# Performance work log

Measured on AMD Instinct MI355X. Metric: run time of the kernel, lower is better.

Reference implementation:

```python
import jax, jax.numpy as jnp
import numpy as np

# NF4 codebook (bitsandbytes values)
NF4_LEVELS = jnp.array([-1.0, -0.6961928009986877, -0.5250730514526367, -0.39491748809814453,
                        -0.28444138169288635, -0.18477343022823334, -0.09105003625154495, 0.0,
                        0.07958029955625534, 0.16093020141124725, 0.24611230194568634,
                        0.33791524171829224, 0.44070982933044434, 0.5626170039176941,
                        0.7229568362236023, 1.0], dtype=jnp.float32)

IN_FEATURES = 4096
OUT_FEATURES = 4096


def setup_inputs() -> dict:
    key = jax.random.key(0)
    k1, k2, k3, k4 = jax.random.split(key, 4)
    x = jax.random.normal(k1, (4, 2048, IN_FEATURES), dtype=jnp.float32)
    # packed uint8 bytes (stored as int32 in [0,256)), shape (O, I//2)
    packed = jax.random.randint(k2, (OUT_FEATURES, IN_FEATURES // 2), 0, 256, dtype=jnp.int32)
    absmax = jax.random.uniform(k3, (OUT_FEATURES,), dtype=jnp.float32) + 1e-3
    bias = jax.random.normal(k4, (OUT_FEATURES,), dtype=jnp.float32)
    return {"x": x, "packed": packed, "absmax": absmax, "bias": bias}


def dequantize_nf4(packed, absmax):
    # packed: (O, I//2) int bytes; high nibble first, then low nibble
    high = (packed >> 4) & 15
    low = packed & 15
    idx = jnp.stack([high, low], axis=2).reshape(packed.shape[0], -1)  # (O, I)
    w = NF4_LEVELS[idx]                    # LUT dequant, (O, I)
    return w * absmax[:, None]             # per-row absmax scaling


def reference(x, packed, absmax, bias):
    # forward: dequantize weight on-the-fly, then F.linear(x, W, bias)
    w = dequantize_nf4(packed, absmax)     # (O, I)
    return jnp.einsum('bsi,oi->bso', x, w) + bias
```

## Files before the change

### kernel.cpp

```cpp
#include <hip/hip_runtime.h>
#include <hip/hip_bf16.h>
#include <stdint.h>

#define M_DIM 8192
#define N_DIM 4096
#define K_DIM 4096

typedef __bf16 bf16_t;
typedef __attribute__((ext_vector_type(8))) __bf16 bf16x8;
typedef __attribute__((ext_vector_type(4))) __bf16 bf16x4;
typedef __attribute__((ext_vector_type(4))) float f32x4;

__constant__ float NF4_LUT[16] = {
    -1.0f, -0.6961928009986877f, -0.5250730514526367f, -0.39491748809814453f,
    -0.28444138169288635f, -0.18477343022823334f, -0.09105003625154495f, 0.0f,
    0.07958029955625534f, 0.16093020141124725f, 0.24611230194568634f,
    0.33791524171829224f, 0.44070982933044434f, 0.5626170039176941f,
    0.7229568362236023f, 1.0f};

__global__ __launch_bounds__(256) void dequant_nf4_kernel(
    const int* __restrict__ packed, const float* __restrict__ absmax,
    bf16_t* __restrict__ W) {
  const int t = blockIdx.x * 256 + threadIdx.x;
  const int row = t >> 9;
  const int c = t & 511;
  const int lane = threadIdx.x & 63;
  const int lutbits = __float_as_int(NF4_LUT[lane & 15]);

  const int4 p = ((const int4*)packed)[t];
  const float am = absmax[row];
  bf16x8 v;
#pragma unroll
  for (int q = 0; q < 4; ++q) {
    const int byte = (q == 0 ? p.x : q == 1 ? p.y : q == 2 ? p.z : p.w) & 255;
    const float hi =
        __int_as_float(__builtin_amdgcn_ds_bpermute(((byte >> 4) & 15) << 2, lutbits));
    const float lo =
        __int_as_float(__builtin_amdgcn_ds_bpermute((byte & 15) << 2, lutbits));
    v[2 * q] = (bf16_t)(hi * am);
    v[2 * q + 1] = (bf16_t)(lo * am);
  }
  *((bf16x8*)&W[(size_t)row * K_DIM + c * 8]) = v;
}

__global__ __launch_bounds__(256) void cvt_bf16_kernel(
    const float* __restrict__ x, bf16_t* __restrict__ y) {
  const int t = blockIdx.x * 256 + threadIdx.x;
  const float4 a = ((const float4*)x)[t];
  bf16x4 v;
  v[0] = (bf16_t)a.x; v[1] = (bf16_t)a.y; v[2] = (bf16_t)a.z; v[3] = (bf16_t)a.w;
  *((bf16x4*)&y[(size_t)t * 4]) = v;
}

#define GLD_LDS16(g, l)                                                     \
  __builtin_amdgcn_global_load_lds(                                        \
      (const __attribute__((address_space(1))) void*)(g),                   \
      (__attribute__((address_space(3))) void*)(l), 16, 0, 0)

__global__ __launch_bounds__(256) void gemm_nf4_kernel(
    const bf16_t* __restrict__ A, const bf16_t* __restrict__ B,
    const float* __restrict__ bias, float* __restrict__ C) {
  constexpr int BM = 128, BN = 128, BK = 32;
  __shared__ __align__(16) bf16_t sA[BM * BK];
  __shared__ __align__(16) bf16_t sB[BN * BK];

  const int tid = threadIdx.x;
  const int wave = tid >> 6, lane = tid & 63;
  const int wr = wave >> 1, wc = wave & 1;
  const int quad = lane >> 4, l15 = lane & 15;

  const int blockM = blockIdx.y * BM;
  const int blockN = blockIdx.x * BN;

  const int sr = tid >> 2;
  const int sk = ((tid & 3) ^ ((tid >> 3) & 3)) * 8;
  const bf16_t* gA0 = A + (size_t)(blockM + sr) * K_DIM + sk;
  const bf16_t* gA1 = gA0 + (size_t)64 * K_DIM;
  const bf16_t* gB0 = B + (size_t)(blockN + sr) * K_DIM + sk;
  const bf16_t* gB1 = gB0 + (size_t)64 * K_DIM;
  bf16_t* lA0 = &sA[tid * 8];
  bf16_t* lA1 = &sA[(tid + 256) * 8];
  bf16_t* lB0 = &sB[tid * 8];
  bf16_t* lB1 = &sB[(tid + 256) * 8];

  f32x4 acc[4][4];
#pragma unroll
  for (int i = 0; i < 4; ++i)
#pragma unroll
    for (int j = 0; j < 4; ++j) acc[i][j] = (f32x4)(0.0f);

  const int cphys = quad ^ ((l15 >> 1) & 3);

  for (int k0 = 0; k0 < K_DIM; k0 += BK) {
    GLD_LDS16(gA0 + k0, lA0);
    GLD_LDS16(gA1 + k0, lA1);
    GLD_LDS16(gB0 + k0, lB0);
    GLD_LDS16(gB1 + k0, lB1);
    __syncthreads();

    bf16x8 af[4], bfr[4];
#pragma unroll
    for (int i = 0; i < 4; ++i) {
      const int rr = wr * 64 + i * 16 + l15;
      af[i] = *(const bf16x8*)&sA[(rr * 4 + cphys) * 8];
    }
#pragma unroll
    for (int j = 0; j < 4; ++j) {
      const int rr = wc * 64 + j * 16 + l15;
      bfr[j] = *(const bf16x8*)&sB[(rr * 4 + cphys) * 8];
    }

#pragma unroll
    for (int i = 0; i < 4; ++i)
#pragma unroll
      for (int j = 0; j < 4; ++j)
        acc[i][j] = __builtin_amdgcn_mfma_f32_16x16x32_bf16(af[i], bfr[j],
                                                            acc[i][j], 0, 0, 0);
    __syncthreads();
  }

#pragma unroll
  for (int j = 0; j < 4; ++j) {
    const int n = blockN + wc * 64 + j * 16 + l15;
    const float bv = bias[n];
#pragma unroll
    for (int i = 0; i < 4; ++i) {
      const int m0 = blockM + wr * 64 + i * 16 + quad * 4;
      f32x4 v = acc[i][j];
      C[(size_t)(m0 + 0) * N_DIM + n] = v[0] + bv;
      C[(size_t)(m0 + 1) * N_DIM + n] = v[1] + bv;
      C[(size_t)(m0 + 2) * N_DIM + n] = v[2] + bv;
      C[(size_t)(m0 + 3) * N_DIM + n] = v[3] + bv;
    }
  }
}

__global__ __launch_bounds__(256) void fallback_kernel(
    const float* __restrict__ x, const int* __restrict__ packed,
    const float* __restrict__ absmax, const float* __restrict__ bias,
    float* __restrict__ out) {
  const int idx = blockIdx.x * 256 + threadIdx.x;
  const int m = idx / N_DIM, n = idx % N_DIM;
  const int* prow = packed + (size_t)n * (K_DIM / 2);
  const float* xr = x + (size_t)m * K_DIM;
  float s = 0.0f;
  for (int p = 0; p < K_DIM / 2; ++p) {
    const int b = prow[p] & 255;
    s += xr[2 * p] * NF4_LUT[(b >> 4) & 15] + xr[2 * p + 1] * NF4_LUT[b & 15];
  }
  out[idx] = s * absmax[n] + bias[n];
}

extern "C" void kernel_launch(void* const* d_in, const int* in_sizes, int n_in,
                              void* d_out, int out_size, void* d_ws,
                              size_t ws_size, hipStream_t stream) {
  const float* x = (const float*)d_in[0];
  const int* packed = (const int*)d_in[1];
  const float* absmax = (const float*)d_in[2];
  const float* bias = (const float*)d_in[3];
  float* out = (float*)d_out;

  const size_t wBytes = (size_t)N_DIM * K_DIM * sizeof(bf16_t);
  const size_t xBytes = (size_t)M_DIM * K_DIM * sizeof(bf16_t);
  if (ws_size < wBytes + xBytes) {
    fallback_kernel<<<dim3((M_DIM * N_DIM) / 256), dim3(256), 0, stream>>>(
        x, packed, absmax, bias, out);
    return;
  }

  bf16_t* W = (bf16_t*)d_ws;
  bf16_t* xb = (bf16_t*)((char*)d_ws + wBytes);

  dequant_nf4_kernel<<<dim3((N_DIM * (K_DIM / 2) / 4) / 256), dim3(256), 0,
                       stream>>>(packed, absmax, W);
  cvt_bf16_kernel<<<dim3((M_DIM * K_DIM / 4) / 256), dim3(256), 0, stream>>>(
      x, xb);
  gemm_nf4_kernel<<<dim3(N_DIM / 128, M_DIM / 128), dim3(256), 0, stream>>>(
      xb, W, bias, out);
}
```

Measured before the change: 543.0 us.

## Rewrite GEMM as 256x256 tile, 8-wave, double-buffered LDS pipeline

Replaces the 128x128x32 single-buffer GEMM with a 256x256x64 tile on 512 threads (8 waves, 2x4 layout). LDS is double-buffered: half-tiles for step t+1 and t+2 are prefetched with global_load_lds while the MFMAs work on the current tile, and the phases are separated by explicit barriers, waitcnts and setprio. It also adds a grouped block-index remap for L2 locality and XOR swizzling of LDS. The aim is to hide load latency and raise arithmetic intensity per tile. In exchange it uses 128KB of LDS, more registers (128 accumulators per lane), and fragile hand-tuned synchronisation.

Result: faster. 527.9 us (-2.8%).

```diff
diff --git a/kernel.cpp b/kernel.cpp
--- a/kernel.cpp
+++ b/kernel.cpp
@@ -57,76 +57,205 @@
       (const __attribute__((address_space(1))) void*)(g),                   \
       (__attribute__((address_space(3))) void*)(l), 16, 0, 0)
 
-__global__ __launch_bounds__(256) void gemm_nf4_kernel(
+#define MFMA_BF16(a, b, c) \
+  __builtin_amdgcn_mfma_f32_16x16x32_bf16((a), (b), (c), 0, 0, 0)
+
+#define STAGE_A1(tt, lds)                                    \
+  do {                                                       \
+    GLD_LDS16(gA1a + (size_t)(tt) * 64, (lds) + dA0);        \
+    GLD_LDS16(gA1b + (size_t)(tt) * 64, (lds) + dA0 + 16384);\
+  } while (0)
+#define STAGE_A2(tt, lds)                                    \
+  do {                                                       \
+    GLD_LDS16(gA2a + (size_t)(tt) * 64, (lds) + dA0 + 8192); \
+    GLD_LDS16(gA2b + (size_t)(tt) * 64, (lds) + dA0 + 24576);\
+  } while (0)
+#define STAGE_B1(tt, lds)                                    \
+  do {                                                       \
+    GLD_LDS16(gB1a + (size_t)(tt) * 64, (lds) + dB0);        \
+    GLD_LDS16(gB1b + (size_t)(tt) * 64, (lds) + dB0 + 16384);\
+  } while (0)
+#define STAGE_B2(tt, lds)                                    \
+  do {                                                       \
+    GLD_LDS16(gB2a + (size_t)(tt) * 64, (lds) + dB0 + 4096); \
+    GLD_LDS16(gB2b + (size_t)(tt) * 64, (lds) + dB0 + 20480);\
+  } while (0)
+
+#define END_BARRIER()                \
+  asm volatile("" ::: "memory");     \
+  __builtin_amdgcn_s_barrier();      \
+  asm volatile("" ::: "memory")
+
+#define MID_BARRIER()                                   \
+  asm volatile("" ::: "memory");                        \
+  __builtin_amdgcn_s_barrier();                         \
+  asm volatile("s_waitcnt lgkmcnt(0)" ::: "memory");    \
+  __builtin_amdgcn_sched_barrier(0)
+
+__global__ __launch_bounds__(512, 2) void gemm_nf4_kernel(
     const bf16_t* __restrict__ A, const bf16_t* __restrict__ B,
     const float* __restrict__ bias, float* __restrict__ C) {
-  constexpr int BM = 128, BN = 128, BK = 32;
-  __shared__ __align__(16) bf16_t sA[BM * BK];
-  __shared__ __align__(16) bf16_t sB[BN * BK];
+  constexpr int NT = K_DIM / 64;
+  __shared__ __align__(16) bf16_t sA[2][256 * 64];
+  __shared__ __align__(16) bf16_t sB[2][256 * 64];
 
   const int tid = threadIdx.x;
   const int wave = tid >> 6, lane = tid & 63;
-  const int wr = wave >> 1, wc = wave & 1;
-  const int quad = lane >> 4, l15 = lane & 15;
-
-  const int blockM = blockIdx.y * BM;
-  const int blockN = blockIdx.x * BN;
-
-  const int sr = tid >> 2;
-  const int sk = ((tid & 3) ^ ((tid >> 3) & 3)) * 8;
-  const bf16_t* gA0 = A + (size_t)(blockM + sr) * K_DIM + sk;
-  const bf16_t* gA1 = gA0 + (size_t)64 * K_DIM;
-  const bf16_t* gB0 = B + (size_t)(blockN + sr) * K_DIM + sk;
-  const bf16_t* gB1 = gB0 + (size_t)64 * K_DIM;
-  bf16_t* lA0 = &sA[tid * 8];
-  bf16_t* lA1 = &sA[(tid + 256) * 8];
-  bf16_t* lB0 = &sB[tid * 8];
-  bf16_t* lB1 = &sB[(tid + 256) * 8];
-
-  f32x4 acc[4][4];
-#pragma unroll
-  for (int i = 0; i < 4; ++i)
+  const int wm = wave >> 2, wn = wave & 3;
+  const int quad = lane >> 4, l15 = lane & 15, l7 = lane & 7;
+
+  const int id = (blockIdx.x & 7) * 64 + (blockIdx.x >> 3);
+  const int blockM = (id & 31) * 256;
+  const int blockN = (id >> 5) * 256;
+
+  const int rqa = tid >> 3;
+  const int cira = ((tid & 7) ^ (rqa & 7)) * 8;
+  const bf16_t* gA1a = A + (size_t)(blockM + rqa) * K_DIM + cira;
+  const bf16_t* gA1b = gA1a + (size_t)128 * K_DIM;
+  const bf16_t* gA2a = gA1a + (size_t)64 * K_DIM;
+  const bf16_t* gA2b = gA1a + (size_t)192 * K_DIM;
+  const int s0 = tid >> 8, cis = tid & 255;
+  const int rqb = cis >> 3;
+  const int cirb = ((cis & 7) ^ (rqb & 7)) * 8;
+  const bf16_t* gB1a = B + (size_t)(blockN + s0 * 64 + rqb) * K_DIM + cirb;
+  const bf16_t* gB1b = gB1a + (size_t)128 * K_DIM;
+  const bf16_t* gB2a = gB1a + (size_t)32 * K_DIM;
+  const bf16_t* gB2b = gB1a + (size_t)160 * K_DIM;
+  const int dA0 = tid * 16;
+  const int dB0 = s0 * 8192 + cis * 16;
+
+  const int aRd0 = wm * 16384 + l15 * 128 + ((quad ^ l7) * 16);
+  const int aRd1 = wm * 16384 + l15 * 128 + (((4 | quad) ^ l7) * 16);
+  const int bRd0 = wn * 8192 + l15 * 128 + ((quad ^ l7) * 16);
+  const int bRd1 = wn * 8192 + l15 * 128 + (((4 | quad) ^ l7) * 16);
+
+  f32x4 acc[8][4];
+#pragma unroll
+  for (int i = 0; i < 8; ++i)
 #pragma unroll
     for (int j = 0; j < 4; ++j) acc[i][j] = (f32x4)(0.0f);
 
-  const int cphys = quad ^ ((l15 >> 1) & 3);
-
-  for (int k0 = 0; k0 < K_DIM; k0 += BK) {
-    GLD_LDS16(gA0 + k0, lA0);
-    GLD_LDS16(gA1 + k0, lA1);
-    GLD_LDS16(gB0 + k0, lB0);
-    GLD_LDS16(gB1 + k0, lB1);
-    __syncthreads();
-
-    bf16x8 af[4], bfr[4];
+  {
+    char* sa0 = (char*)sA[0];
+    char* sb0 = (char*)sB[0];
+    char* sa1 = (char*)sA[1];
+    char* sb1 = (char*)sB[1];
+    STAGE_A1(0, sa0);
+    STAGE_B1(0, sb0);
+    STAGE_A2(0, sa0);
+    STAGE_B2(0, sb0);
+    STAGE_A1(1, sa1);
+    STAGE_B1(1, sb1);
+    asm volatile("s_waitcnt vmcnt(4)" ::: "memory");
+    __builtin_amdgcn_s_barrier();
+    asm volatile("" ::: "memory");
+  }
+
+  for (int t = 0; t < NT; ++t) {
+    char* sa = (char*)sA[t & 1];
+    char* sao = (char*)sA[(t + 1) & 1];
+    char* sb = (char*)sB[t & 1];
+    char* sbo = (char*)sB[(t + 1) & 1];
+
+    bf16x8 af[4][2], bq[2][2];
+
 #pragma unroll
     for (int i = 0; i < 4; ++i) {
-      const int rr = wr * 64 + i * 16 + l15;
-      af[i] = *(const bf16x8*)&sA[(rr * 4 + cphys) * 8];
-    }
-#pragma unroll
-    for (int j = 0; j < 4; ++j) {
-      const int rr = wc * 64 + j * 16 + l15;
-      bfr[j] = *(const bf16x8*)&sB[(rr * 4 + cphys) * 8];
-    }
-
+      af[i][0] = *(const bf16x8*)(sa + aRd0 + i * 2048);
+      af[i][1] = *(const bf16x8*)(sa + aRd1 + i * 2048);
+    }
+#pragma unroll
+    for (int j = 0; j < 2; ++j) {
+      bq[j][0] = *(const bf16x8*)(sb + bRd0 + j * 2048);
+      bq[j][1] = *(const bf16x8*)(sb + bRd1 + j * 2048);
+    }
+    if (t + 1 < NT) STAGE_A2(t + 1, sao);
+    asm volatile("s_waitcnt lgkmcnt(8)" ::: "memory");
+    MID_BARRIER();
+    __builtin_amdgcn_s_setprio(1);
 #pragma unroll
     for (int i = 0; i < 4; ++i)
 #pragma unroll
-      for (int j = 0; j < 4; ++j)
-        acc[i][j] = __builtin_amdgcn_mfma_f32_16x16x32_bf16(af[i], bfr[j],
-                                                            acc[i][j], 0, 0, 0);
-    __syncthreads();
-  }
-
-#pragma unroll
-  for (int j = 0; j < 4; ++j) {
-    const int n = blockN + wc * 64 + j * 16 + l15;
+      for (int j = 0; j < 2; ++j) {
+        acc[i][j] = MFMA_BF16(af[i][0], bq[j][0], acc[i][j]);
+        acc[i][j] = MFMA_BF16(af[i][1], bq[j][1], acc[i][j]);
+      }
+    __builtin_amdgcn_s_setprio(0);
+    END_BARRIER();
+
+#pragma unroll
+    for (int j = 0; j < 2; ++j) {
+      bq[j][0] = *(const bf16x8*)(sb + bRd0 + (2 + j) * 2048);
+      bq[j][1] = *(const bf16x8*)(sb + bRd1 + (2 + j) * 2048);
+    }
+    if (t + 1 < NT) STAGE_B2(t + 1, sbo);
+    MID_BARRIER();
+    __builtin_amdgcn_s_setprio(1);
+#pragma unroll
+    for (int i = 0; i < 4; ++i)
+#pragma unroll
+      for (int j = 0; j < 2; ++j) {
+        acc[i][2 + j] = MFMA_BF16(af[i][0], bq[j][0], acc[i][2 + j]);
+        acc[i][2 + j] = MFMA_BF16(af[i][1], bq[j][1], acc[i][2 + j]);
+      }
+    __builtin_amdgcn_s_setprio(0);
+    END_BARRIER();
+
+#pragma unroll
+    for (int i = 0; i < 4; ++i) {
+      af[i][0] = *(const bf16x8*)(sa + aRd0 + (4 + i) * 2048);
+      af[i][1] = *(const bf16x8*)(sa + aRd1 + (4 + i) * 2048);
+    }
+#pragma unroll
+    for (int j = 0; j < 2; ++j) {
+      bq[j][0] = *(const bf16x8*)(sb + bRd0 + j * 2048);
+      bq[j][1] = *(const bf16x8*)(sb + bRd1 + j * 2048);
+    }
+    if (t + 2 < NT) STAGE_A1(t + 2, sa);
+    asm volatile("s_waitcnt lgkmcnt(8)" ::: "memory");
+    MID_BARRIER();
+    __builtin_amdgcn_s_setprio(1);
+#pragma unroll
+    for (int i = 0; i < 4; ++i)
+#pragma unroll
+      for (int j = 0; j < 2; ++j) {
+        acc[4 + i][j] = MFMA_BF16(af[i][0], bq[j][0], acc[4 + i][j]);
+        acc[4 + i][j] = MFMA_BF16(af[i][1], bq[j][1], acc[4 + i][j]);
+      }
+    __builtin_amdgcn_s_setprio(0);
+    END_BARRIER();
+
+#pragma unroll
+    for (int j = 0; j < 2; ++j) {
+      bq[j][0] = *(const bf16x8*)(sb + bRd0 + (2 + j) * 2048);
+      bq[j][1] = *(const bf16x8*)(sb + bRd1 + (2 + j) * 2048);
+    }
+    if (t + 2 < NT) STAGE_B1(t + 2, sb);
+    MID_BARRIER();
+    __builtin_amdgcn_s_setprio(1);
+#pragma unroll
+    for (int i = 0; i < 4; ++i)
+#pragma unroll
+      for (int j = 0; j < 2; ++j) {
+        acc[4 + i][2 + j] = MFMA_BF16(af[i][0], bq[j][0], acc[4 + i][2 + j]);
+        acc[4 + i][2 + j] = MFMA_BF16(af[i][1], bq[j][1], acc[4 + i][2 + j]);
+      }
+    __builtin_amdgcn_s_setprio(0);
+    if (t < NT - 2)
+      asm volatile("s_waitcnt vmcnt(4)" ::: "memory");
+    else
+      asm volatile("s_waitcnt vmcnt(0)" ::: "memory");
+    END_BARRIER();
+  }
+
+#pragma unroll
+  for (int nf = 0; nf < 4; ++nf) {
+    const int n = blockN + wn * 64 + nf * 16 + l15;
     const float bv = bias[n];
 #pragma unroll
-    for (int i = 0; i < 4; ++i) {
-      const int m0 = blockM + wr * 64 + i * 16 + quad * 4;
-      f32x4 v = acc[i][j];
+    for (int mf = 0; mf < 8; ++mf) {
+      const int m0 = blockM + wm * 128 + mf * 16 + quad * 4;
+      f32x4 v = acc[mf][nf];
       C[(size_t)(m0 + 0) * N_DIM + n] = v[0] + bv;
       C[(size_t)(m0 + 1) * N_DIM + n] = v[1] + bv;
       C[(size_t)(m0 + 2) * N_DIM + n] = v[2] + bv;
@@ -175,6 +304,6 @@
                        stream>>>(packed, absmax, W);
   cvt_bf16_kernel<<<dim3((M_DIM * K_DIM / 4) / 256), dim3(256), 0, stream>>>(
       x, xb);
-  gemm_nf4_kernel<<<dim3(N_DIM / 128, M_DIM / 128), dim3(256), 0, stream>>>(
-      xb, W, bias, out);
-}
+  gemm_nf4_kernel<<<dim3((M_DIM / 256) * (N_DIM / 256)), dim3(512), 0,
+                    stream>>>(xb, W, bias, out);
+}
```
